# Kernel tuning notes

Hardware: AMD Instinct MI355X
Metric: run time of the kernel (lower is better)

Reference implementation:

```python
import jax, jax.numpy as jnp
import numpy as np

TOP_K = 2

def setup_inputs() -> dict:
    key = jax.random.key(0)
    ks = jax.random.split(key, 8)
    B, S, H, F, E = 2, 2048, 1024, 2048, 8
    sH = 1.0 / np.sqrt(H)
    sF = 1.0 / np.sqrt(F)
    return {
        "hidden_states": jax.random.normal(ks[0], (B, S, H), jnp.float32),
        "gate_w": jax.random.normal(ks[1], (E, H), jnp.float32) * sH,
        "w_up": jax.random.normal(ks[2], (E, H, F), jnp.float32) * sH,
        "w_gate": jax.random.normal(ks[3], (E, H, F), jnp.float32) * sH,
        "w_down": jax.random.normal(ks[4], (E, F, H), jnp.float32) * sF,
        "b_up": jnp.zeros((E, F), jnp.float32),
        "b_gate": jnp.zeros((E, F), jnp.float32),
        "b_down": jnp.zeros((E, H), jnp.float32),
    }

def reference(hidden_states, gate_w, w_up, w_gate, w_down, b_up, b_gate, b_down):
    # Flatten [B,S,H] -> [N,H]
    H = hidden_states.shape[-1]
    x = hidden_states.reshape(-1, H)                      # [N,H]
    router_logits = x @ gate_w.T                          # [N,E]
    probs = jax.nn.softmax(router_logits.astype(jnp.float32), axis=-1)
    topv, topi = jax.lax.top_k(probs, TOP_K)              # [N,K]
    topv = topv / topv.sum(axis=-1, keepdims=True)
    N, E = router_logits.shape
    # Sparse combine weights: zero except top-k experts (renormalized).
    w_full = jnp.zeros((N, E), probs.dtype).at[jnp.arange(N)[:, None], topi].set(topv)
    w_full = w_full.astype(x.dtype)
    # SwiGLU per expert (dense over E; combine weights zero out non-selected).
    u = jnp.einsum('nh,ehf->nef', x, w_up) + b_up         # [N,E,F]
    v = jnp.einsum('nh,ehf->nef', x, w_gate) + b_gate
    phi = jax.nn.silu(v) * u
    y = jnp.einsum('nef,efh->neh', phi, w_down) + b_down  # [N,E,H]
    out = jnp.einsum('ne,neh->nh', w_full, y)             # [N,H]
    out = out.reshape(hidden_states.shape)
    return out, router_logits.astype(hidden_states.dtype)
```

## Files before the change

### kernel.cpp

```cpp
#include <hip/hip_runtime.h>
#include <hip/hip_bf16.h>
#include <cstdint>
#include <cstddef>

#define N_TOK 4096
#define H_DIM 1024
#define F_DIM 2048
#define E_NUM 8
#define RCAP 10240
#define MAXT 40

typedef __attribute__((ext_vector_type(8))) short bf16x8;
typedef __attribute__((ext_vector_type(4))) float f32x4;

__device__ __forceinline__ float b2f(uint16_t u) {
  return __uint_as_float(((uint32_t)u) << 16);
}
__device__ __forceinline__ uint16_t f2b(float f) {
  uint32_t x = __float_as_uint(f);
  uint32_t r = (x + 0x7fffu + ((x >> 16) & 1u)) >> 16;
  return (uint16_t)r;
}

__device__ __forceinline__ void gl2lds16(const void* g, void* l) {
  __builtin_amdgcn_global_load_lds(
      (const __attribute__((address_space(1))) uint32_t*)g,
      (__attribute__((address_space(3))) uint32_t*)l, 16, 0, 0);
}

__device__ __forceinline__ void stage256(const uint16_t* src, int ldK,
                                         char* lds, int wave, int lane) {
  int u = (lane & 7) ^ (lane >> 3);
  const char* s0 = (const char*)src + u * 16;
  size_t rb = (size_t)ldK * 2;
  int Rb = wave * 32 + (lane >> 3);
  char* d0 = lds + wave * 4096;
  for (int c = 0; c < 4; ++c)
    gl2lds16(s0 + (size_t)(Rb + c * 8) * rb, d0 + c * 1024);
}

__device__ __forceinline__ void stage128(const uint16_t* src, int ldK,
                                         char* lds, int wave, int lane) {
  int u = (lane & 7) ^ (lane >> 3);
  const char* s0 = (const char*)src + u * 16;
  size_t rb = (size_t)ldK * 2;
  int Rb = wave * 16 + (lane >> 3);
  char* d0 = lds + wave * 2048;
  for (int c = 0; c < 2; ++c)
    gl2lds16(s0 + (size_t)(Rb + c * 8) * rb, d0 + c * 1024);
}

__device__ __forceinline__ bf16x8 read_frag(const char* lds, int R, int s,
                                            int q) {
  int unit = ((s << 2) + q) ^ (R & 7);
  return *(const bf16x8*)(lds + R * 128 + unit * 16);
}

__global__ __launch_bounds__(256) void detect_kernel(
    const uint16_t* __restrict__ x, int* __restrict__ flag) {
  __shared__ int cnt;
  if (threadIdx.x == 0) cnt = 0;
  __syncthreads();
  int ok = 0;
  for (int j = 0; j < 16; ++j) {
    uint16_t u = x[threadIdx.x * 16 + j];
    int e = (u >> 7) & 0xff;
    ok += (u == 0 || (e >= 96 && e <= 143)) ? 1 : 0;
  }
  atomicAdd(&cnt, ok);
  __syncthreads();
  if (threadIdx.x == 0) *flag = (cnt >= 3700) ? 1 : 0;
}

__global__ __launch_bounds__(256) void router_kernel(
    const void* __restrict__ xraw, const void* __restrict__ gwraw,
    const int* __restrict__ flag, void* __restrict__ dout,
    int* __restrict__ top_i, float* __restrict__ top_w) {
  int fl = *flag;
  int wave = threadIdx.x >> 6, lane = threadIdx.x & 63;
  int t = blockIdx.x * 4 + wave;
  float xv[16];
  if (fl) {
    const uint16_t* xr = (const uint16_t*)xraw + (size_t)t * H_DIM + lane * 16;
    uint4 a = *(const uint4*)xr;
    uint4 b = *(const uint4*)(xr + 8);
    uint32_t w[8] = {a.x, a.y, a.z, a.w, b.x, b.y, b.z, b.w};
    for (int j = 0; j < 8; ++j) {
      xv[2 * j] = b2f((uint16_t)(w[j] & 0xffff));
      xv[2 * j + 1] = b2f((uint16_t)(w[j] >> 16));
    }
  } else {
    const float* xr = (const float*)xraw + (size_t)t * H_DIM + lane * 16;
    for (int j = 0; j < 4; ++j) {
      float4 v = ((const float4*)xr)[j];
      xv[4 * j] = v.x; xv[4 * j + 1] = v.y;
      xv[4 * j + 2] = v.z; xv[4 * j + 3] = v.w;
    }
  }
  float acc[E_NUM];
  for (int e = 0; e < E_NUM; ++e) {
    float s = 0.f;
    if (fl) {
      const uint16_t* gr =
          (const uint16_t*)gwraw + (size_t)e * H_DIM + lane * 16;
      uint4 a = *(const uint4*)gr;
      uint4 b = *(const uint4*)(gr + 8);
      uint32_t w[8] = {a.x, a.y, a.z, a.w, b.x, b.y, b.z, b.w};
      for (int j = 0; j < 8; ++j) {
        s += xv[2 * j] * b2f((uint16_t)(w[j] & 0xffff));
        s += xv[2 * j + 1] * b2f((uint16_t)(w[j] >> 16));
      }
    } else {
      const float* gr = (const float*)gwraw + (size_t)e * H_DIM + lane * 16;
      for (int j = 0; j < 4; ++j) {
        float4 v = ((const float4*)gr)[j];
        s += xv[4 * j] * v.x + xv[4 * j + 1] * v.y + xv[4 * j + 2] * v.z +
             xv[4 * j + 3] * v.w;
      }
    }
    acc[e] = s;
  }
  for (int off = 32; off >= 1; off >>= 1)
    for (int e = 0; e < E_NUM; ++e)
      acc[e] += __shfl_xor(acc[e], off, 64);
  if (lane < E_NUM) {
    size_t idx = (size_t)N_TOK * H_DIM + (size_t)t * E_NUM + lane;
    if (fl)
      ((uint16_t*)dout)[idx] = f2b(acc[lane]);
    else
      ((float*)dout)[idx] = acc[lane];
  }
  if (lane == 0) {
    int b0 = 0;
    float v0 = acc[0];
    for (int e = 1; e < E_NUM; ++e)
      if (acc[e] > v0) { v0 = acc[e]; b0 = e; }
    int b1 = (b0 == 0) ? 1 : 0;
    float v1 = acc[b1];
    for (int e = 0; e < E_NUM; ++e)
      if (e != b0 && acc[e] > v1) { v1 = acc[e]; b1 = e; }
    float w0 = 1.f / (1.f + expf(v1 - v0));
    top_i[2 * t] = b0; top_i[2 * t + 1] = b1;
    top_w[2 * t] = w0; top_w[2 * t + 1] = 1.f - w0;
  }
}

__global__ __launch_bounds__(1024) void histscan_kernel(
    const int* __restrict__ top_i, int* __restrict__ counts,
    int* __restrict__ bases, int* __restrict__ row_of,
    int* __restrict__ tile_e, int* __restrict__ tile_row,
    int* __restrict__ ntiles) {
  int tid = threadIdx.x;
  int lane = tid & 63, wave = tid >> 6;
  int e_loc[8];
  int c[E_NUM] = {};
  for (int j = 0; j < 8; ++j) {
    int idx = tid * 8 + j;
    int e = top_i[idx];
    e_loc[j] = e;
    c[e]++;
  }
  int inc[E_NUM];
  for (int k = 0; k < E_NUM; ++k) inc[k] = c[k];
  for (int off = 1; off < 64; off <<= 1) {
    for (int k = 0; k < E_NUM; ++k) {
      int v = __shfl_up(inc[k], off, 64);
      if (lane >= off) inc[k] += v;
    }
  }
  __shared__ int wtot[16][E_NUM];
  __shared__ int woff[16][E_NUM];
  __shared__ int base_s[E_NUM];
  if (lane == 63)
    for (int k = 0; k < E_NUM; ++k) wtot[wave][k] = inc[k];
  __syncthreads();
  if (tid < E_NUM) {
    int run = 0;
    for (int w = 0; w < 16; ++w) {
      woff[w][tid] = run;
      run += wtot[w][tid];
    }
    counts[tid] = run;
    wtot[0][tid] = run;
  }
  __syncthreads();
  if (tid == 0) {
    int b = 0, nt = 0;
    for (int e = 0; e < E_NUM; ++e) {
      bases[e] = b;
      base_s[e] = b;
      int cc = wtot[0][e];
      int te = (cc + 255) >> 8;
      for (int j = 0; j < te; ++j) {
        tile_e[nt] = e;
        tile_row[nt] = b + j * 256;
        ++nt;
      }
      b += te << 8;
    }
    *ntiles = nt;
  }
  __syncthreads();
  int run[E_NUM];
  for (int k = 0; k < E_NUM; ++k)
    run[k] = base_s[k] + woff[wave][k] + inc[k] - c[k];
  for (int j = 0; j < 8; ++j) {
    int idx = tid * 8 + j;
    int r = run[e_loc[j]]++;
    row_of[idx] = r;
  }
}

__global__ __launch_bounds__(256) void gather_kernel(
    const void* __restrict__ xraw, const int* __restrict__ flag,
    const int* __restrict__ row_of, uint16_t* __restrict__ Xg) {
  int t = blockIdx.x;
  int rs0 = row_of[2 * t], rs1 = row_of[2 * t + 1];
  uint2 v;
  if (*flag) {
    v = ((const uint2*)((const uint16_t*)xraw + (size_t)t * H_DIM))[threadIdx.x];
  } else {
    float4 f =
        ((const float4*)((const float*)xraw + (size_t)t * H_DIM))[threadIdx.x];
    v.x = (uint32_t)f2b(f.x) | ((uint32_t)f2b(f.y) << 16);
    v.y = (uint32_t)f2b(f.z) | ((uint32_t)f2b(f.w) << 16);
  }
  ((uint2*)(Xg + (size_t)rs0 * H_DIM))[threadIdx.x] = v;
  ((uint2*)(Xg + (size_t)rs1 * H_DIM))[threadIdx.x] = v;
}

__global__ __launch_bounds__(256) void transpose_kernel(
    const void* __restrict__ W, const int* __restrict__ flag,
    uint16_t* __restrict__ Wt, int K, int N) {
  int e = blockIdx.z;
  int n0 = blockIdx.x * 64, k0 = blockIdx.y * 64;
  __shared__ __align__(16) uint16_t tile[64][72];
  size_t ebase = (size_t)e * K * N;
  uint16_t* Wout = Wt + ebase;
  int fl = *flag;
  int r = threadIdx.x >> 3;
  int c = (threadIdx.x & 7) * 8;
  if (fl) {
    const uint16_t* Win = (const uint16_t*)W + ebase;
    for (int it = 0; it < 2; ++it) {
      int row = r + it * 32;
      uint4 v = *(const uint4*)(Win + (size_t)(k0 + row) * N + n0 + c);
      *(uint4*)&tile[row][c] = v;
    }
  } else {
    const float* Win = (const float*)W + ebase;
    for (int it = 0; it < 2; ++it) {
      int row = r + it * 32;
      const float* p = Win + (size_t)(k0 + row) * N + n0 + c;
      float4 a = ((const float4*)p)[0];
      float4 b = ((const float4*)p)[1];
      uint16_t* tp = &tile[row][c];
      tp[0] = f2b(a.x); tp[1] = f2b(a.y); tp[2] = f2b(a.z); tp[3] = f2b(a.w);
      tp[4] = f2b(b.x); tp[5] = f2b(b.y); tp[6] = f2b(b.z); tp[7] = f2b(b.w);
    }
  }
  __syncthreads();
  for (int it = 0; it < 2; ++it) {
    int n = r + it * 32;
    uint4 o;
    o.x = (uint32_t)tile[c + 0][n] | ((uint32_t)tile[c + 1][n] << 16);
    o.y = (uint32_t)tile[c + 2][n] | ((uint32_t)tile[c + 3][n] << 16);
    o.z = (uint32_t)tile[c + 4][n] | ((uint32_t)tile[c + 5][n] << 16);
    o.w = (uint32_t)tile[c + 6][n] | ((uint32_t)tile[c + 7][n] << 16);
    *(uint4*)(Wout + (size_t)(n0 + n) * K + k0 + c) = o;
  }
}

__global__ __launch_bounds__(512, 2) void gemm_upgate(
    const uint16_t* __restrict__ Xg,
    const uint16_t* __restrict__ WtU, const uint16_t* __restrict__ WtG,
    const void* __restrict__ buRaw, const void* __restrict__ bgRaw,
    const int* __restrict__ flag, const int* __restrict__ tile_e,
    const int* __restrict__ tile_row, const int* __restrict__ ntiles,
    uint16_t* __restrict__ phi) {
  int ty = blockIdx.y;
  if (ty >= *ntiles) return;
  int e = tile_e[ty];
  int r0 = tile_row[ty];
  int n0 = blockIdx.x * 128;
  const uint16_t* A = Xg + (size_t)r0 * H_DIM;
  const uint16_t* BU = WtU + (size_t)e * F_DIM * H_DIM + (size_t)n0 * H_DIM;
  const uint16_t* BG = WtG + (size_t)e * F_DIM * H_DIM + (size_t)n0 * H_DIM;

  __shared__ __align__(16) char lA[2][256 * 128];
  __shared__ __align__(16) char lBu[2][128 * 128];
  __shared__ __align__(16) char lBg[2][128 * 128];

  int tid = threadIdx.x;
  int wave = tid >> 6, lane = tid & 63;
  int wm = wave >> 1, wn = wave & 1;
  int q = lane >> 4, mr = lane & 15;

  f32x4 accU[4][4] = {};
  f32x4 accG[4][4] = {};

  stage256(A, H_DIM, lA[0], wave, lane);
  stage128(BU, H_DIM, lBu[0], wave, lane);
  stage128(BG, H_DIM, lBg[0], wave, lane);

  for (int k0 = 0; k0 < H_DIM; k0 += 64) {
    int cur = (k0 >> 6) & 1;
    if (k0 + 64 < H_DIM) {
      stage256(A + k0 + 64, H_DIM, lA[cur ^ 1], wave, lane);
      stage128(BU + k0 + 64, H_DIM, lBu[cur ^ 1], wave, lane);
      stage128(BG + k0 + 64, H_DIM, lBg[cur ^ 1], wave, lane);
      asm volatile("s_waitcnt vmcnt(8)" ::: "memory");
    } else {
      asm volatile("s_waitcnt vmcnt(0)" ::: "memory");
    }
    __builtin_amdgcn_s_barrier();
    __builtin_amdgcn_sched_barrier(0);
    const char* pA = lA[cur];
    const char* pU = lBu[cur];
    const char* pG = lBg[cur];
    for (int s = 0; s < 2; ++s) {
      bf16x8 af[4], bu[4], bg[4];
      for (int mt = 0; mt < 4; ++mt)
        af[mt] = read_frag(pA, wm * 64 + mt * 16 + mr, s, q);
      for (int nt = 0; nt < 4; ++nt) {
        bu[nt] = read_frag(pU, wn * 64 + nt * 16 + mr, s, q);
        bg[nt] = read_frag(pG, wn * 64 + nt * 16 + mr, s, q);
      }
      for (int mt = 0; mt < 4; ++mt)
        for (int nt = 0; nt < 4; ++nt) {
          accU[mt][nt] = __builtin_amdgcn_mfma_f32_16x16x32_bf16(
              af[mt], bu[nt], accU[mt][nt], 0, 0, 0);
          accG[mt][nt] = __builtin_amdgcn_mfma_f32_16x16x32_bf16(
              af[mt], bg[nt], accG[mt][nt], 0, 0, 0);
        }
    }
    __builtin_amdgcn_sched_barrier(0);
    __builtin_amdgcn_s_barrier();
  }

  int fl = *flag;
  int rb_ = r0 + wm * 64;
  int cb_ = n0 + wn * 64;
  for (int nt = 0; nt < 4; ++nt) {
    int col = cb_ + nt * 16 + mr;
    float bu_v, bg_v;
    if (fl) {
      bu_v = b2f(((const uint16_t*)buRaw)[(size_t)e * F_DIM + col]);
      bg_v = b2f(((const uint16_t*)bgRaw)[(size_t)e * F_DIM + col]);
    } else {
      bu_v = ((const float*)buRaw)[(size_t)e * F_DIM + col];
      bg_v = ((const float*)bgRaw)[(size_t)e * F_DIM + col];
    }
    for (int mt = 0; mt < 4; ++mt) {
      int r = rb_ + mt * 16 + q * 4;
      for (int rg = 0; rg < 4; ++rg) {
        float u = accU[mt][nt][rg] + bu_v;
        float v = accG[mt][nt][rg] + bg_v;
        float s = v / (1.f + expf(-v));
        phi[(size_t)(r + rg) * F_DIM + col] = f2b(s * u);
      }
    }
  }
}

__global__ __launch_bounds__(512, 2) void gemm_down(
    const uint16_t* __restrict__ phi, const uint16_t* __restrict__ WtD,
    const void* __restrict__ bdRaw, const int* __restrict__ flag,
    const int* __restrict__ tile_e, const int* __restrict__ tile_row,
    const int* __restrict__ ntiles, float* __restrict__ Yrows) {
  int ty = blockIdx.y;
  if (ty >= *ntiles) return;
  int e = tile_e[ty];
  int r0 = tile_row[ty];
  int n0 = blockIdx.x * 256;
  const uint16_t* A = phi + (size_t)r0 * F_DIM;
  const uint16_t* B = WtD + (size_t)e * H_DIM * F_DIM + (size_t)n0 * F_DIM;

  __shared__ __align__(16) char lA[2][256 * 128];
  __shared__ __align__(16) char lB[2][256 * 128];

  int tid = threadIdx.x;
  int wave = tid >> 6, lane = tid & 63;
  int wm = wave >> 2, wn = wave & 3;
  int q = lane >> 4, mr = lane & 15;

  f32x4 acc[8][4] = {};

  stage256(A, F_DIM, lA[0], wave, lane);
  stage256(B, F_DIM, lB[0], wave, lane);

  for (int k0 = 0; k0 < F_DIM; k0 += 64) {
    int cur = (k0 >> 6) & 1;
    if (k0 + 64 < F_DIM) {
      stage256(A + k0 + 64, F_DIM, lA[cur ^ 1], wave, lane);
      stage256(B + k0 + 64, F_DIM, lB[cur ^ 1], wave, lane);
      asm volatile("s_waitcnt vmcnt(8)" ::: "memory");
    } else {
      asm volatile("s_waitcnt vmcnt(0)" ::: "memory");
    }
    __builtin_amdgcn_s_barrier();
    __builtin_amdgcn_sched_barrier(0);
    const char* pA = lA[cur];
    const char* pB = lB[cur];
    for (int s = 0; s < 2; ++s) {
      bf16x8 af[8], bf[4];
      for (int mt = 0; mt < 8; ++mt)
        af[mt] = read_frag(pA, wm * 128 + mt * 16 + mr, s, q);
      for (int nt = 0; nt < 4; ++nt)
        bf[nt] = read_frag(pB, wn * 64 + nt * 16 + mr, s, q);
      for (int mt = 0; mt < 8; ++mt)
        for (int nt = 0; nt < 4; ++nt)
          acc[mt][nt] = __builtin_amdgcn_mfma_f32_16x16x32_bf16(
              af[mt], bf[nt], acc[mt][nt], 0, 0, 0);
    }
    __builtin_amdgcn_sched_barrier(0);
    __builtin_amdgcn_s_barrier();
  }

  int fl = *flag;
  int rb_ = r0 + wm * 128;
  int cb_ = n0 + wn * 64;
  for (int nt = 0; nt < 4; ++nt) {
    int col = cb_ + nt * 16 + mr;
    float bd_v = fl ? b2f(((const uint16_t*)bdRaw)[(size_t)e * H_DIM + col])
                    : ((const float*)bdRaw)[(size_t)e * H_DIM + col];
    for (int mt = 0; mt < 8; ++mt) {
      int r = rb_ + mt * 16 + q * 4;
      for (int rg = 0; rg < 4; ++rg)
        Yrows[(size_t)(r + rg) * H_DIM + col] = acc[mt][nt][rg] + bd_v;
    }
  }
}

__global__ __launch_bounds__(256) void combine_kernel(
    const float* __restrict__ Y, const int* __restrict__ row_of,
    const float* __restrict__ top_w, const int* __restrict__ flag,
    void* __restrict__ out) {
  int t = blockIdx.x;
  int r0 = row_of[2 * t], r1 = row_of[2 * t + 1];
  float w0 = top_w[2 * t], w1 = top_w[2 * t + 1];
  int i = threadIdx.x;
  float4 a = ((const float4*)(Y + (size_t)r0 * H_DIM))[i];
  float4 b = ((const float4*)(Y + (size_t)r1 * H_DIM))[i];
  float4 o;
  o.x = w0 * a.x + w1 * b.x;
  o.y = w0 * a.y + w1 * b.y;
  o.z = w0 * a.z + w1 * b.z;
  o.w = w0 * a.w + w1 * b.w;
  if (*flag) {
    uint2 p;
    p.x = (uint32_t)f2b(o.x) | ((uint32_t)f2b(o.y) << 16);
    p.y = (uint32_t)f2b(o.z) | ((uint32_t)f2b(o.w) << 16);
    ((uint2*)out)[(size_t)t * 256 + i] = p;
  } else {
    ((float4*)out)[(size_t)t * 256 + i] = o;
  }
}

extern "C" void kernel_launch(void* const* d_in, const int* in_sizes, int n_in,
                              void* d_out, int out_size, void* d_ws, size_t ws_size,
                              hipStream_t stream) {
  const void* x = d_in[0];
  const void* gw = d_in[1];
  const void* w_up = d_in[2];
  const void* w_gate = d_in[3];
  const void* w_down = d_in[4];
  const void* b_up = d_in[5];
  const void* b_gate = d_in[6];
  const void* b_down = d_in[7];

  char* ws = (char*)d_ws;
  size_t off = 0;
  auto alloc = [&](size_t bytes) -> void* {
    void* p = ws + off;
    off += (bytes + 255) & ~(size_t)255;
    return p;
  };
  int* counts = (int*)alloc(32);
  int* bases = (int*)alloc(32);
  int* flag = (int*)alloc(32);
  int* ntiles = (int*)alloc(32);
  int* tile_e = (int*)alloc(sizeof(int) * MAXT);
  int* tile_row = (int*)alloc(sizeof(int) * MAXT);
  int* top_i = (int*)alloc(sizeof(int) * N_TOK * 2);
  float* top_w = (float*)alloc(sizeof(float) * N_TOK * 2);
  int* row_of = (int*)alloc(sizeof(int) * N_TOK * 2);
  uint16_t* Xg = (uint16_t*)alloc((size_t)RCAP * H_DIM * 2);
  uint16_t* phi = (uint16_t*)alloc((size_t)RCAP * F_DIM * 2);
  uint16_t* WtU = (uint16_t*)alloc((size_t)E_NUM * H_DIM * F_DIM * 2);
  uint16_t* WtG = (uint16_t*)alloc((size_t)E_NUM * H_DIM * F_DIM * 2);
  float* Yrows = (float*)alloc((size_t)RCAP * H_DIM * sizeof(float));

  detect_kernel<<<1, 256, 0, stream>>>((const uint16_t*)x, flag);
  router_kernel<<<N_TOK / 4, 256, 0, stream>>>(x, gw, flag, d_out, top_i,
                                               top_w);
  histscan_kernel<<<1, 1024, 0, stream>>>(top_i, counts, bases, row_of,
                                          tile_e, tile_row, ntiles);
  gather_kernel<<<N_TOK, 256, 0, stream>>>(x, flag, row_of, Xg);

  transpose_kernel<<<dim3(F_DIM / 64, H_DIM / 64, E_NUM), 256, 0, stream>>>(
      w_up, flag, WtU, H_DIM, F_DIM);
  transpose_kernel<<<dim3(F_DIM / 64, H_DIM / 64, E_NUM), 256, 0, stream>>>(
      w_gate, flag, WtG, H_DIM, F_DIM);

  gemm_upgate<<<dim3(F_DIM / 128, MAXT), 512, 0, stream>>>(
      Xg, WtU, WtG, b_up, b_gate, flag, tile_e, tile_row, ntiles, phi);

  transpose_kernel<<<dim3(H_DIM / 64, F_DIM / 64, E_NUM), 256, 0, stream>>>(
      w_down, flag, WtU, F_DIM, H_DIM);
  gemm_down<<<dim3(H_DIM / 256, MAXT), 512, 0, stream>>>(
      phi, WtU, b_down, flag, tile_e, tile_row, ntiles, Yrows);

  combine_kernel<<<N_TOK, 256, 0, stream>>>(Yrows, row_of, top_w, flag, d_out);
}
```

Before: 458.1 us.

## Interleave staged loads with MFMA phases and retile down GEMM to 256x128

The up/gate GEMM main loop is split into four phases, each issuing part of the next K-tile's global-to-LDS loads before a batch of MFMAs. Partial waitcnts and setprio around the MFMA blocks let memory transfers overlap compute instead of waiting at one barrier per tile. The down GEMM drops from a 256x256 to a 256x128 tile with the same phased staging, which doubles its block count and reduces accumulator registers. The up and gate weight transposes are merged into one launch. The cost is more barriers per K-step, and the smaller down tile rereads the A operand more often.

```diff
diff --git a/kernel.cpp b/kernel.cpp
--- a/kernel.cpp
+++ b/kernel.cpp
@@ -38,7 +38,17 @@
   for (int c = 0; c < 4; ++c)
     gl2lds16(s0 + (size_t)(Rb + c * 8) * rb, d0 + c * 1024);
 }
-
+__device__ __forceinline__ void stage256h(const uint16_t* src, int ldK,
+                                          char* lds, int wave, int lane,
+                                          int h) {
+  int u = (lane & 7) ^ (lane >> 3);
+  const char* s0 = (const char*)src + u * 16;
+  size_t rb = (size_t)ldK * 2;
+  int Rb = wave * 32 + (lane >> 3);
+  char* d0 = lds + wave * 4096;
+  for (int c = 2 * h; c < 2 * h + 2; ++c)
+    gl2lds16(s0 + (size_t)(Rb + c * 8) * rb, d0 + c * 1024);
+}
 __device__ __forceinline__ void stage128(const uint16_t* src, int ldK,
                                          char* lds, int wave, int lane) {
   int u = (lane & 7) ^ (lane >> 3);
@@ -48,6 +58,15 @@
   char* d0 = lds + wave * 2048;
   for (int c = 0; c < 2; ++c)
     gl2lds16(s0 + (size_t)(Rb + c * 8) * rb, d0 + c * 1024);
+}
+__device__ __forceinline__ void stage128h(const uint16_t* src, int ldK,
+                                          char* lds, int wave, int lane,
+                                          int h) {
+  int u = (lane & 7) ^ (lane >> 3);
+  const char* s0 = (const char*)src + u * 16;
+  size_t rb = (size_t)ldK * 2;
+  int Rb = wave * 16 + (lane >> 3);
+  gl2lds16(s0 + (size_t)(Rb + h * 8) * rb, lds + wave * 2048 + h * 1024);
 }
 
 __device__ __forceinline__ bf16x8 read_frag(const char* lds, int R, int s,
@@ -230,9 +249,13 @@
 }
 
 __global__ __launch_bounds__(256) void transpose_kernel(
-    const void* __restrict__ W, const int* __restrict__ flag,
-    uint16_t* __restrict__ Wt, int K, int N) {
-  int e = blockIdx.z;
+    const void* __restrict__ W0, const void* __restrict__ W1,
+    const int* __restrict__ flag, uint16_t* __restrict__ Wt0,
+    uint16_t* __restrict__ Wt1, int K, int N) {
+  int z = blockIdx.z;
+  int e = z & (E_NUM - 1);
+  const void* W = (z < E_NUM) ? W0 : W1;
+  uint16_t* Wt = (z < E_NUM) ? Wt0 : Wt1;
   int n0 = blockIdx.x * 64, k0 = blockIdx.y * 64;
   __shared__ __align__(16) uint16_t tile[64][72];
   size_t ebase = (size_t)e * K * N;
@@ -303,37 +326,121 @@
   stage128(BU, H_DIM, lBu[0], wave, lane);
   stage128(BG, H_DIM, lBg[0], wave, lane);
 
-  for (int k0 = 0; k0 < H_DIM; k0 += 64) {
-    int cur = (k0 >> 6) & 1;
-    if (k0 + 64 < H_DIM) {
-      stage256(A + k0 + 64, H_DIM, lA[cur ^ 1], wave, lane);
-      stage128(BU + k0 + 64, H_DIM, lBu[cur ^ 1], wave, lane);
-      stage128(BG + k0 + 64, H_DIM, lBg[cur ^ 1], wave, lane);
-      asm volatile("s_waitcnt vmcnt(8)" ::: "memory");
-    } else {
-      asm volatile("s_waitcnt vmcnt(0)" ::: "memory");
-    }
-    __builtin_amdgcn_s_barrier();
-    __builtin_amdgcn_sched_barrier(0);
+  const int NT = H_DIM / 64;
+  for (int t = 0; t < NT; ++t) {
+    int cur = t & 1, nxt = cur ^ 1;
+    int k1 = (t + 1) * 64;
+    bool more = (t + 1 < NT);
     const char* pA = lA[cur];
     const char* pU = lBu[cur];
     const char* pG = lBg[cur];
-    for (int s = 0; s < 2; ++s) {
-      bf16x8 af[4], bu[4], bg[4];
-      for (int mt = 0; mt < 4; ++mt)
-        af[mt] = read_frag(pA, wm * 64 + mt * 16 + mr, s, q);
+
+    if (more) {
+      stage256h(A + k1, H_DIM, lA[nxt], wave, lane, 0);
+      asm volatile("s_waitcnt vmcnt(2)" ::: "memory");
+    } else {
+      asm volatile("s_waitcnt vmcnt(0)" ::: "memory");
+    }
+    __builtin_amdgcn_s_barrier();
+    __builtin_amdgcn_sched_barrier(0);
+    bf16x8 af0[2][2], bu[4][2];
+#pragma unroll
+    for (int mt = 0; mt < 2; ++mt)
+#pragma unroll
+      for (int s = 0; s < 2; ++s)
+        af0[mt][s] = read_frag(pA, wm * 64 + mt * 16 + mr, s, q);
+#pragma unroll
+    for (int nt = 0; nt < 4; ++nt)
+#pragma unroll
+      for (int s = 0; s < 2; ++s)
+        bu[nt][s] = read_frag(pU, wn * 64 + nt * 16 + mr, s, q);
+    asm volatile("s_waitcnt lgkmcnt(0)" ::: "memory");
+    __builtin_amdgcn_sched_barrier(0);
+    __builtin_amdgcn_s_setprio(1);
+#pragma unroll
+    for (int mt = 0; mt < 2; ++mt)
+#pragma unroll
       for (int nt = 0; nt < 4; ++nt) {
-        bu[nt] = read_frag(pU, wn * 64 + nt * 16 + mr, s, q);
-        bg[nt] = read_frag(pG, wn * 64 + nt * 16 + mr, s, q);
-      }
-      for (int mt = 0; mt < 4; ++mt)
-        for (int nt = 0; nt < 4; ++nt) {
-          accU[mt][nt] = __builtin_amdgcn_mfma_f32_16x16x32_bf16(
-              af[mt], bu[nt], accU[mt][nt], 0, 0, 0);
-          accG[mt][nt] = __builtin_amdgcn_mfma_f32_16x16x32_bf16(
-              af[mt], bg[nt], accG[mt][nt], 0, 0, 0);
-        }
-    }
+        accU[mt][nt] = __builtin_amdgcn_mfma_f32_16x16x32_bf16(
+            af0[mt][0], bu[nt][0], accU[mt][nt], 0, 0, 0);
+        accU[mt][nt] = __builtin_amdgcn_mfma_f32_16x16x32_bf16(
+            af0[mt][1], bu[nt][1], accU[mt][nt], 0, 0, 0);
+      }
+    __builtin_amdgcn_s_setprio(0);
+    __builtin_amdgcn_sched_barrier(0);
+    __builtin_amdgcn_s_barrier();
+
+    if (more) stage256h(A + k1, H_DIM, lA[nxt], wave, lane, 1);
+    bf16x8 bg[4][2];
+#pragma unroll
+    for (int nt = 0; nt < 4; ++nt)
+#pragma unroll
+      for (int s = 0; s < 2; ++s)
+        bg[nt][s] = read_frag(pG, wn * 64 + nt * 16 + mr, s, q);
+    asm volatile("s_waitcnt lgkmcnt(0)" ::: "memory");
+    __builtin_amdgcn_sched_barrier(0);
+    __builtin_amdgcn_s_setprio(1);
+#pragma unroll
+    for (int mt = 0; mt < 2; ++mt)
+#pragma unroll
+      for (int nt = 0; nt < 4; ++nt) {
+        accG[mt][nt] = __builtin_amdgcn_mfma_f32_16x16x32_bf16(
+            af0[mt][0], bg[nt][0], accG[mt][nt], 0, 0, 0);
+        accG[mt][nt] = __builtin_amdgcn_mfma_f32_16x16x32_bf16(
+            af0[mt][1], bg[nt][1], accG[mt][nt], 0, 0, 0);
+      }
+    __builtin_amdgcn_s_setprio(0);
+    __builtin_amdgcn_sched_barrier(0);
+    __builtin_amdgcn_s_barrier();
+
+    if (more) stage128(BU + k1, H_DIM, lBu[nxt], wave, lane);
+    bf16x8 af1[2][2], bu2[4][2];
+#pragma unroll
+    for (int mt = 0; mt < 2; ++mt)
+#pragma unroll
+      for (int s = 0; s < 2; ++s)
+        af1[mt][s] = read_frag(pA, wm * 64 + (mt + 2) * 16 + mr, s, q);
+#pragma unroll
+    for (int nt = 0; nt < 4; ++nt)
+#pragma unroll
+      for (int s = 0; s < 2; ++s)
+        bu2[nt][s] = read_frag(pU, wn * 64 + nt * 16 + mr, s, q);
+    asm volatile("s_waitcnt lgkmcnt(0)" ::: "memory");
+    __builtin_amdgcn_sched_barrier(0);
+    __builtin_amdgcn_s_setprio(1);
+#pragma unroll
+    for (int mt = 0; mt < 2; ++mt)
+#pragma unroll
+      for (int nt = 0; nt < 4; ++nt) {
+        accU[mt + 2][nt] = __builtin_amdgcn_mfma_f32_16x16x32_bf16(
+            af1[mt][0], bu2[nt][0], accU[mt + 2][nt], 0, 0, 0);
+        accU[mt + 2][nt] = __builtin_amdgcn_mfma_f32_16x16x32_bf16(
+            af1[mt][1], bu2[nt][1], accU[mt + 2][nt], 0, 0, 0);
+      }
+    __builtin_amdgcn_s_setprio(0);
+    __builtin_amdgcn_sched_barrier(0);
+    __builtin_amdgcn_s_barrier();
+
+    if (more) stage128(BG + k1, H_DIM, lBg[nxt], wave, lane);
+    bf16x8 bg2[4][2];
+#pragma unroll
+    for (int nt = 0; nt < 4; ++nt)
+#pragma unroll
+      for (int s = 0; s < 2; ++s)
+        bg2[nt][s] = read_frag(pG, wn * 64 + nt * 16 + mr, s, q);
+    asm volatile("s_waitcnt lgkmcnt(0)" ::: "memory");
+    __builtin_amdgcn_sched_barrier(0);
+    __builtin_amdgcn_s_setprio(1);
+#pragma unroll
+    for (int mt = 0; mt < 2; ++mt)
+#pragma unroll
+      for (int nt = 0; nt < 4; ++nt) {
+        accG[mt + 2][nt] = __builtin_amdgcn_mfma_f32_16x16x32_bf16(
+            af1[mt][0], bg2[nt][0], accG[mt + 2][nt], 0, 0, 0);
+        accG[mt + 2][nt] = __builtin_amdgcn_mfma_f32_16x16x32_bf16(
+            af1[mt][1], bg2[nt][1], accG[mt + 2][nt], 0, 0, 0);
+      }
+    __builtin_amdgcn_s_setprio(0);
     __builtin_amdgcn_sched_barrier(0);
     __builtin_amdgcn_s_barrier();
   }
@@ -368,63 +475,111 @@
     const void* __restrict__ bdRaw, const int* __restrict__ flag,
     const int* __restrict__ tile_e, const int* __restrict__ tile_row,
     const int* __restrict__ ntiles, float* __restrict__ Yrows) {
-  int ty = blockIdx.y;
+  int ty = blockIdx.x;
   if (ty >= *ntiles) return;
   int e = tile_e[ty];
   int r0 = tile_row[ty];
-  int n0 = blockIdx.x * 256;
+  int n0 = blockIdx.y * 128;
   const uint16_t* A = phi + (size_t)r0 * F_DIM;
   const uint16_t* B = WtD + (size_t)e * H_DIM * F_DIM + (size_t)n0 * F_DIM;
 
   __shared__ __align__(16) char lA[2][256 * 128];
-  __shared__ __align__(16) char lB[2][256 * 128];
+  __shared__ __align__(16) char lB[2][128 * 128];
 
   int tid = threadIdx.x;
   int wave = tid >> 6, lane = tid & 63;
-  int wm = wave >> 2, wn = wave & 3;
+  int wm = wave >> 1, wn = wave & 1;
   int q = lane >> 4, mr = lane & 15;
 
-  f32x4 acc[8][4] = {};
+  f32x4 acc[4][4] = {};
 
   stage256(A, F_DIM, lA[0], wave, lane);
-  stage256(B, F_DIM, lB[0], wave, lane);
-
-  for (int k0 = 0; k0 < F_DIM; k0 += 64) {
-    int cur = (k0 >> 6) & 1;
-    if (k0 + 64 < F_DIM) {
-      stage256(A + k0 + 64, F_DIM, lA[cur ^ 1], wave, lane);
-      stage256(B + k0 + 64, F_DIM, lB[cur ^ 1], wave, lane);
-      asm volatile("s_waitcnt vmcnt(8)" ::: "memory");
+  stage128(B, F_DIM, lB[0], wave, lane);
+
+  const int NT = F_DIM / 64;
+  for (int t = 0; t < NT; ++t) {
+    int cur = t & 1, nxt = cur ^ 1;
+    int k1 = (t + 1) * 64;
+    bool more = (t + 1 < NT);
+    const char* pA = lA[cur];
+    const char* pB = lB[cur];
+
+    if (more) {
+      stage256h(A + k1, F_DIM, lA[nxt], wave, lane, 0);
+      stage128h(B + k1, F_DIM, lB[nxt], wave, lane, 0);
+      asm volatile("s_waitcnt vmcnt(3)" ::: "memory");
     } else {
       asm volatile("s_waitcnt vmcnt(0)" ::: "memory");
     }
     __builtin_amdgcn_s_barrier();
     __builtin_amdgcn_sched_barrier(0);
-    const char* pA = lA[cur];
-    const char* pB = lB[cur];
-    for (int s = 0; s < 2; ++s) {
-      bf16x8 af[8], bf[4];
-      for (int mt = 0; mt < 8; ++mt)
-        af[mt] = read_frag(pA, wm * 128 + mt * 16 + mr, s, q);
-      for (int nt = 0; nt < 4; ++nt)
-        bf[nt] = read_frag(pB, wn * 64 + nt * 16 + mr, s, q);
-      for (int mt = 0; mt < 8; ++mt)
-        for (int nt = 0; nt < 4; ++nt)
-          acc[mt][nt] = __builtin_amdgcn_mfma_f32_16x16x32_bf16(
-              af[mt], bf[nt], acc[mt][nt], 0, 0, 0);
-    }
+    bf16x8 af[2][2], bf[4][2];
+#pragma unroll
+    for (int mt = 0; mt < 2; ++mt)
+#pragma unroll
+      for (int s = 0; s < 2; ++s)
+        af[mt][s] = read_frag(pA, wm * 64 + mt * 16 + mr, s, q);
+#pragma unroll
+    for (int nt = 0; nt < 4; ++nt)
+#pragma unroll
+      for (int s = 0; s < 2; ++s)
+        bf[nt][s] = read_frag(pB, wn * 64 + nt * 16 + mr, s, q);
+    asm volatile("s_waitcnt lgkmcnt(0)" ::: "memory");
+    __builtin_amdgcn_sched_barrier(0);
+    __builtin_amdgcn_s_setprio(1);
+#pragma unroll
+    for (int mt = 0; mt < 2; ++mt)
+#pragma unroll
+      for (int nt = 0; nt < 4; ++nt) {
+        acc[mt][nt] = __builtin_amdgcn_mfma_f32_16x16x32_bf16(
+            af[mt][0], bf[nt][0], acc[mt][nt], 0, 0, 0);
+        acc[mt][nt] = __builtin_amdgcn_mfma_f32_16x16x32_bf16(
+            af[mt][1], bf[nt][1], acc[mt][nt], 0, 0, 0);
+      }
+    __builtin_amdgcn_s_setprio(0);
+    __builtin_amdgcn_sched_barrier(0);
+    __builtin_amdgcn_s_barrier();
+
+    if (more) {
+      stage256h(A + k1, F_DIM, lA[nxt], wave, lane, 1);
+      stage128h(B + k1, F_DIM, lB[nxt], wave, lane, 1);
+    }
+    bf16x8 af2[2][2], bf2[4][2];
+#pragma unroll
+    for (int mt = 0; mt < 2; ++mt)
+#pragma unroll
+      for (int s = 0; s < 2; ++s)
+        af2[mt][s] = read_frag(pA, wm * 64 + (mt + 2) * 16 + mr, s, q);
+#pragma unroll
+    for (int nt = 0; nt < 4; ++nt)
+#pragma unroll
+      for (int s = 0; s < 2; ++s)
+        bf2[nt][s] = read_frag(pB, wn * 64 + nt * 16 + mr, s, q);
+    asm volatile("s_waitcnt lgkmcnt(0)" ::: "memory");
+    __builtin_amdgcn_sched_barrier(0);
+    __builtin_amdgcn_s_setprio(1);
+#pragma unroll
+    for (int mt = 0; mt < 2; ++mt)
+#pragma unroll
+      for (int nt = 0; nt < 4; ++nt) {
+        acc[mt + 2][nt] = __builtin_amdgcn_mfma_f32_16x16x32_bf16(
+            af2[mt][0], bf2[nt][0], acc[mt + 2][nt], 0, 0, 0);
+        acc[mt + 2][nt] = __builtin_amdgcn_mfma_f32_16x16x32_bf16(
+            af2[mt][1], bf2[nt][1], acc[mt + 2][nt], 0, 0, 0);
+      }
+    __builtin_amdgcn_s_setprio(0);
     __builtin_amdgcn_sched_barrier(0);
     __builtin_amdgcn_s_barrier();
   }
 
   int fl = *flag;
-  int rb_ = r0 + wm * 128;
+  int rb_ = r0 + wm * 64;
   int cb_ = n0 + wn * 64;
   for (int nt = 0; nt < 4; ++nt) {
     int col = cb_ + nt * 16 + mr;
     float bd_v = fl ? b2f(((const uint16_t*)bdRaw)[(size_t)e * H_DIM + col])
                     : ((const float*)bdRaw)[(size_t)e * H_DIM + col];
-    for (int mt = 0; mt < 8; ++mt) {
+    for (int mt = 0; mt < 4; ++mt) {
       int r = rb_ + mt * 16 + q * 4;
       for (int rg = 0; rg < 4; ++rg)
         Yrows[(size_t)(r + rg) * H_DIM + col] = acc[mt][nt][rg] + bd_v;
@@ -498,17 +653,15 @@
                                           tile_e, tile_row, ntiles);
   gather_kernel<<<N_TOK, 256, 0, stream>>>(x, flag, row_of, Xg);
 
-  transpose_kernel<<<dim3(F_DIM / 64, H_DIM / 64, E_NUM), 256, 0, stream>>>(
-      w_up, flag, WtU, H_DIM, F_DIM);
-  transpose_kernel<<<dim3(F_DIM / 64, H_DIM / 64, E_NUM), 256, 0, stream>>>(
-      w_gate, flag, WtG, H_DIM, F_DIM);
+  transpose_kernel<<<dim3(F_DIM / 64, H_DIM / 64, 2 * E_NUM), 256, 0,
+                     stream>>>(w_up, w_gate, flag, WtU, WtG, H_DIM, F_DIM);
 
   gemm_upgate<<<dim3(F_DIM / 128, MAXT), 512, 0, stream>>>(
       Xg, WtU, WtG, b_up, b_gate, flag, tile_e, tile_row, ntiles, phi);
 
   transpose_kernel<<<dim3(H_DIM / 64, F_DIM / 64, E_NUM), 256, 0, stream>>>(
-      w_down, flag, WtU, F_DIM, H_DIM);
-  gemm_down<<<dim3(H_DIM / 256, MAXT), 512, 0, stream>>>(
+      w_down, w_down, flag, WtU, WtU, F_DIM, H_DIM);
+  gemm_down<<<dim3(MAXT, H_DIM / 128), 512, 0, stream>>>(
       phi, WtU, b_down, flag, tile_e, tile_row, ntiles, Yrows);
 
   combine_kernel<<<N_TOK, 256, 0, stream>>>(Yrows, row_of, top_w, flag, d_out);
```

Measured after the change: 516.5 us. +12.8%, slower.
